# Optimization experiments

Hardware: AMD Instinct MI355X
Metric: run time of the kernel (lower is better)

## Reference

```python
import jax, jax.numpy as jnp
import numpy as np

T, H, I, E = 2048, 2048, 1024, 16
TOP_K = 4

def setup_inputs() -> dict:
    key = jax.random.key(0)
    k1, k2, k3, k4, k5 = jax.random.split(key, 5)
    scale = 0.02
    return {
        "hidden_states": jax.random.normal(k1, (T, H), dtype=jnp.float32),
        "gate_w": jax.random.normal(k2, (E, H), dtype=jnp.float32) * scale,
        "w1": jax.random.normal(k3, (E, H, I), dtype=jnp.float32) * scale,  # gate proj
        "w3": jax.random.normal(k4, (E, H, I), dtype=jnp.float32) * scale,  # up proj
        "w2": jax.random.normal(k5, (E, I, H), dtype=jnp.float32) * scale,  # down proj
    }

def reference(hidden_states, gate_w, w1, w3, w2):
    # Router gate in fp32 (ReplicatedLinear, params_dtype=fp32, no bias)
    logits = hidden_states.astype(jnp.float32) @ gate_w.T          # [T, E]
    scores = jax.nn.softmax(logits, axis=-1)                        # scoring_func=softmax
    topk_w, topk_idx = jax.lax.top_k(scores, TOP_K)                 # [T, K]
    # renormalize=True, routed_scaling_factor=1.0
    topk_w = topk_w / jnp.sum(topk_w, axis=-1, keepdims=True)
    # Dense combine weights [T, E]: zero for non-selected experts, so
    # the dense all-expert compute below is mathematically identical to
    # sparse dispatch + grouped GEMM + combine.
    tok = jnp.arange(T)[:, None]
    cw = jnp.zeros((T, E), jnp.float32).at[tok, topk_idx].add(topk_w)
    # SwiGLU expert MLPs
    h1 = jnp.einsum('th,ehi->eti', hidden_states, w1)               # [E, T, I]
    h3 = jnp.einsum('th,ehi->eti', hidden_states, w3)               # [E, T, I]
    h2 = jnp.einsum('eti,eih->eth', jax.nn.silu(h1) * h3, w2)       # [E, T, H]
    out = jnp.einsum('te,eth->th', cw.astype(hidden_states.dtype), h2)
    return out
```

## Files before the change

### kernel.cpp

```cpp
#include <hip/hip_runtime.h>
#include <hip/hip_bf16.h>
#include <math.h>

#define T_TOK 2048
#define H_DIM 2048
#define I_DIM 1024
#define E_NUM 16
#define TOPK  4

#define BM 128
#define BN 128
#define BK 32
#define MAXMB 80

typedef __attribute__((ext_vector_type(8))) __bf16 bf16x8;
typedef __attribute__((ext_vector_type(4))) float  f32x4;

__device__ __forceinline__ unsigned short f2bf(float f) {
    unsigned int u = __builtin_bit_cast(unsigned int, f);
    unsigned int r = u + 0x7FFFu + ((u >> 16) & 1u);
    return (unsigned short)(r >> 16);
}

__device__ __forceinline__ void gload16(const void* g, void* l) {
    __builtin_amdgcn_global_load_lds(
        (const __attribute__((address_space(1))) unsigned int*)g,
        (__attribute__((address_space(3))) unsigned int*)l,
        16, 0, 0);
}

static const size_t WS_COUNTS  = 0;
static const size_t WS_WORK    = 64;
static const size_t WS_OFFSETS = 256;
static const size_t WS_TOK     = 512;
static const size_t WS_WL      = 131584;
static const size_t WS_X16     = 262656;
static const size_t WS_W1T     = 8651264;
static const size_t WS_W3T     = 75760128;
static const size_t WS_W2T     = 142868992;
static const size_t WS_ACT     = 209977856;


__global__ void zero_init(float* __restrict__ out, int* __restrict__ counts) {
    int i = blockIdx.x * blockDim.x + threadIdx.x;
    ((float4*)out)[i] = make_float4(0.f, 0.f, 0.f, 0.f);
    if (i < E_NUM) counts[i] = 0;
}

__global__ void convert_x(const float* __restrict__ x, unsigned short* __restrict__ X16) {
    int i = blockIdx.x * blockDim.x + threadIdx.x;
    float4 v = ((const float4*)x)[i];
    ushort4 o;
    o.x = f2bf(v.x); o.y = f2bf(v.y); o.z = f2bf(v.z); o.w = f2bf(v.w);
    ((ushort4*)X16)[i] = o;
}

__global__ void transpose_conv(const float* __restrict__ in, unsigned short* __restrict__ out,
                               int R, int C) {
    __shared__ unsigned short tile[32][33];
    int e  = blockIdx.z;
    int c0 = blockIdx.x * 32;
    int r0 = blockIdx.y * 32;
    const float* ip = in + (size_t)e * R * C;
    unsigned short* op = out + (size_t)e * R * C;
    int t = threadIdx.x;
    int r  = t >> 3;
    int c4 = (t & 7) * 4;
    float4 v = *(const float4*)&ip[(size_t)(r0 + r) * C + c0 + c4];
    tile[c4 + 0][r] = f2bf(v.x);
    tile[c4 + 1][r] = f2bf(v.y);
    tile[c4 + 2][r] = f2bf(v.z);
    tile[c4 + 3][r] = f2bf(v.w);
    __syncthreads();
    ushort4 o;
    o.x = tile[r][c4 + 0];
    o.y = tile[r][c4 + 1];
    o.z = tile[r][c4 + 2];
    o.w = tile[r][c4 + 3];
    *(ushort4*)&op[(size_t)(c0 + r) * R + r0 + c4] = o;
}

__global__ void router(const float* __restrict__ x, const float* __restrict__ gw,
                       int* __restrict__ counts, int* __restrict__ tok,
                       float* __restrict__ wl) {
    int t = blockIdx.x;
    int lane = threadIdx.x;
    float acc[E_NUM];
#pragma unroll
    for (int e = 0; e < E_NUM; e++) acc[e] = 0.f;
    const float* xr = x + (size_t)t * H_DIM;
    for (int h = lane; h < H_DIM; h += 64) {
        float xv = xr[h];
#pragma unroll
        for (int e = 0; e < E_NUM; e++) acc[e] += xv * gw[e * H_DIM + h];
    }
#pragma unroll
    for (int e = 0; e < E_NUM; e++) {
#pragma unroll
        for (int off = 32; off; off >>= 1) acc[e] += __shfl_down(acc[e], off);
    }
    if (lane == 0) {
        bool used[E_NUM];
#pragma unroll
        for (int e = 0; e < E_NUM; e++) used[e] = false;
        int   idx[TOPK];
        float lv[TOPK];
        for (int k = 0; k < TOPK; k++) {
            float best = -1e30f; int bi = 0;
            for (int e = 0; e < E_NUM; e++)
                if (!used[e] && acc[e] > best) { best = acc[e]; bi = e; }
            used[bi] = true; idx[k] = bi; lv[k] = best;
        }
        float m = lv[0];
        float w[TOPK]; float s = 0.f;
        for (int k = 0; k < TOPK; k++) { w[k] = expf(lv[k] - m); s += w[k]; }
        float inv = 1.f / s;
        for (int k = 0; k < TOPK; k++) {
            int pos = atomicAdd(&counts[idx[k]], 1);
            tok[idx[k] * T_TOK + pos] = t;
            wl [idx[k] * T_TOK + pos] = w[k] * inv;
        }
    }
}

__global__ void prefix(const int* __restrict__ counts, int* __restrict__ offsets,
                       unsigned short* __restrict__ work) {
    if (threadIdx.x == 0 && blockIdx.x == 0) {
        int c[E_NUM]; int s = 0;
        for (int e = 0; e < E_NUM; e++) { c[e] = counts[e]; offsets[e] = s; s += c[e]; }
        offsets[E_NUM] = s;
        int n = 0;
        for (int e = 0; e < E_NUM; e++) {
            int mb = (c[e] + BM - 1) / BM;
            for (int m = 0; m < mb; m++) work[n++] = (unsigned short)((e << 8) | m);
        }
        offsets[E_NUM + 1] = n;
    }
}

__global__ __launch_bounds__(256, 2) void stage1(
    const unsigned short* __restrict__ X16,
    const unsigned short* __restrict__ w1t,
    const unsigned short* __restrict__ w3t,
    const int* __restrict__ offsets, const unsigned short* __restrict__ work,
    const int* __restrict__ tok, const float* __restrict__ wl,
    unsigned short* __restrict__ act)
{
    int j = blockIdx.y;
    if (j >= offsets[E_NUM + 1]) return;
    int ent = work[j];
    int e   = ent >> 8;
    int m0  = (ent & 255) * BM;
    int n_e = offsets[e + 1] - offsets[e];
    int n0  = blockIdx.x * BN;

    __shared__ __align__(16) unsigned short As [BM][BK];
    __shared__ __align__(16) unsigned short B1s[BN][BK];
    __shared__ __align__(16) unsigned short B2s[BN][BK];

    int tid  = threadIdx.x;
    int wave = tid >> 6, lane = tid & 63;
    int wm = (wave >> 1) * 64, wn = (wave & 1) * 64;
    int lr = lane & 15, lq = lane >> 4;

    const unsigned short* w1p = w1t + (size_t)e * I_DIM * H_DIM;
    const unsigned short* w3p = w3t + (size_t)e * I_DIM * H_DIM;

    int ar[2]; int rr[2]; int cc[2];
#pragma unroll
    for (int rep = 0; rep < 2; rep++) {
        int idx = rep * 256 + tid;
        rr[rep] = idx >> 2;
        cc[rep] = (idx & 3) * 8;
        int gm = m0 + rr[rep];
        ar[rep] = tok[e * T_TOK + (gm < n_e ? gm : n_e - 1)];
    }

    f32x4 acc1[4][4] = {};
    f32x4 acc3[4][4] = {};

    for (int k0 = 0; k0 < H_DIM; k0 += BK) {
#pragma unroll
        for (int rep = 0; rep < 2; rep++) {
            int r = rr[rep], ch = cc[rep];
            gload16(&X16[(size_t)ar[rep] * H_DIM + k0 + ch], &As [r][ch]);
            gload16(&w1p[(size_t)(n0 + r) * H_DIM + k0 + ch], &B1s[r][ch]);
            gload16(&w3p[(size_t)(n0 + r) * H_DIM + k0 + ch], &B2s[r][ch]);
        }
        __syncthreads();
        bf16x8 af[4], b1f[4], b2f[4];
#pragma unroll
        for (int ti = 0; ti < 4; ti++)
            af[ti] = *(const bf16x8*)&As[wm + ti * 16 + lr][lq * 8];
#pragma unroll
        for (int tj = 0; tj < 4; tj++) {
            b1f[tj] = *(const bf16x8*)&B1s[wn + tj * 16 + lr][lq * 8];
            b2f[tj] = *(const bf16x8*)&B2s[wn + tj * 16 + lr][lq * 8];
        }
#pragma unroll
        for (int ti = 0; ti < 4; ti++)
#pragma unroll
            for (int tj = 0; tj < 4; tj++) {
                acc1[ti][tj] = __builtin_amdgcn_mfma_f32_16x16x32_bf16(af[ti], b1f[tj], acc1[ti][tj], 0, 0, 0);
                acc3[ti][tj] = __builtin_amdgcn_mfma_f32_16x16x32_bf16(af[ti], b2f[tj], acc3[ti][tj], 0, 0, 0);
            }
        __syncthreads();
    }

    int slotbase = offsets[e] + m0;
#pragma unroll
    for (int ti = 0; ti < 4; ti++) {
#pragma unroll
        for (int reg = 0; reg < 4; reg++) {
            int mrow = wm + ti * 16 + lq * 4 + reg;
            int gm = m0 + mrow;
            if (gm >= n_e) continue;
            float wt = wl[e * T_TOK + gm];
            size_t obase = (size_t)(slotbase + mrow) * I_DIM + n0;
#pragma unroll
            for (int tj = 0; tj < 4; tj++) {
                float h1 = acc1[ti][tj][reg];
                float h3 = acc3[ti][tj][reg];
                float a = (h1 / (1.f + expf(-h1))) * h3 * wt;
                act[obase + wn + tj * 16 + lr] = f2bf(a);
            }
        }
    }
}

__global__ __launch_bounds__(256, 2) void stage2(
    const unsigned short* __restrict__ act,
    const unsigned short* __restrict__ w2t,
    const int* __restrict__ offsets, const unsigned short* __restrict__ work,
    const int* __restrict__ tok,
    float* __restrict__ out)
{
    int j = blockIdx.y;
    if (j >= offsets[E_NUM + 1]) return;
    int ent = work[j];
    int e   = ent >> 8;
    int m0  = (ent & 255) * BM;
    int n_e = offsets[e + 1] - offsets[e];
    int n0  = blockIdx.x * BN;

    __shared__ __align__(16) unsigned short As[BM][BK];
    __shared__ __align__(16) unsigned short Bs[BN][BK];

    int tid  = threadIdx.x;
    int wave = tid >> 6, lane = tid & 63;
    int wm = (wave >> 1) * 64, wn = (wave & 1) * 64;
    int lr = lane & 15, lq = lane >> 4;

    const unsigned short* w2p = w2t + (size_t)e * H_DIM * I_DIM;
    int slotbase = offsets[e];

    int rr[2]; int cc[2]; int arow[2];
#pragma unroll
    for (int rep = 0; rep < 2; rep++) {
        int idx = rep * 256 + tid;
        rr[rep] = idx >> 2;
        cc[rep] = (idx & 3) * 8;
        int gm = m0 + rr[rep];
        arow[rep] = slotbase + (gm < n_e ? gm : n_e - 1);
    }

    f32x4 acc[4][4] = {};

    for (int k0 = 0; k0 < I_DIM; k0 += BK) {
#pragma unroll
        for (int rep = 0; rep < 2; rep++) {
            int r = rr[rep], ch = cc[rep];
            gload16(&act[(size_t)arow[rep] * I_DIM + k0 + ch], &As[r][ch]);
            gload16(&w2p[(size_t)(n0 + r) * I_DIM + k0 + ch], &Bs[r][ch]);
        }
        __syncthreads();
        bf16x8 af[4], bf[4];
#pragma unroll
        for (int ti = 0; ti < 4; ti++)
            af[ti] = *(const bf16x8*)&As[wm + ti * 16 + lr][lq * 8];
#pragma unroll
        for (int tj = 0; tj < 4; tj++)
            bf[tj] = *(const bf16x8*)&Bs[wn + tj * 16 + lr][lq * 8];
#pragma unroll
        for (int ti = 0; ti < 4; ti++)
#pragma unroll
            for (int tj = 0; tj < 4; tj++)
                acc[ti][tj] = __builtin_amdgcn_mfma_f32_16x16x32_bf16(af[ti], bf[tj], acc[ti][tj], 0, 0, 0);
        __syncthreads();
    }

#pragma unroll
    for (int ti = 0; ti < 4; ti++) {
#pragma unroll
        for (int reg = 0; reg < 4; reg++) {
            int mrow = wm + ti * 16 + lq * 4 + reg;
            int gm = m0 + mrow;
            if (gm >= n_e) continue;
            int tm = tok[e * T_TOK + gm];
            size_t obase = (size_t)tm * H_DIM + n0;
#pragma unroll
            for (int tj = 0; tj < 4; tj++)
                atomicAdd(&out[obase + wn + tj * 16 + lr], acc[ti][tj][reg]);
        }
    }
}

extern "C" void kernel_launch(void* const* d_in, const int* in_sizes, int n_in,
                              void* d_out, int out_size, void* d_ws, size_t ws_size,
                              hipStream_t stream) {
    const float* x_f32 = (const float*)d_in[0];
    const float* gw    = (const float*)d_in[1];
    const float* w1    = (const float*)d_in[2];
    const float* w3    = (const float*)d_in[3];
    const float* w2    = (const float*)d_in[4];
    float* out = (float*)d_out;

    char* ws = (char*)d_ws;
    int*            counts  = (int*)(ws + WS_COUNTS);
    unsigned short* work    = (unsigned short*)(ws + WS_WORK);
    int*            offsets = (int*)(ws + WS_OFFSETS);
    int*            tok     = (int*)(ws + WS_TOK);
    float*          wl      = (float*)(ws + WS_WL);
    unsigned short* X16     = (unsigned short*)(ws + WS_X16);
    unsigned short* w1t     = (unsigned short*)(ws + WS_W1T);
    unsigned short* w3t     = (unsigned short*)(ws + WS_W3T);
    unsigned short* w2t     = (unsigned short*)(ws + WS_W2T);
    unsigned short* act     = (unsigned short*)(ws + WS_ACT);

    zero_init<<<dim3((T_TOK * H_DIM / 4) / 256), 256, 0, stream>>>(out, counts);
    convert_x<<<dim3((T_TOK * H_DIM / 4) / 256), 256, 0, stream>>>(x_f32, X16);
    transpose_conv<<<dim3(I_DIM / 32, H_DIM / 32, E_NUM), 256, 0, stream>>>(w1, w1t, H_DIM, I_DIM);
    transpose_conv<<<dim3(I_DIM / 32, H_DIM / 32, E_NUM), 256, 0, stream>>>(w3, w3t, H_DIM, I_DIM);
    transpose_conv<<<dim3(H_DIM / 32, I_DIM / 32, E_NUM), 256, 0, stream>>>(w2, w2t, I_DIM, H_DIM);
    router<<<dim3(T_TOK), 64, 0, stream>>>(x_f32, gw, counts, tok, wl);
    prefix<<<dim3(1), 64, 0, stream>>>(counts, offsets, work);
    stage1<<<dim3(I_DIM / BN, MAXMB), 256, 0, stream>>>(
        X16, w1t, w3t, offsets, work, tok, wl, act);
    stage2<<<dim3(H_DIM / BN, MAXMB), 256, 0, stream>>>(
        act, w2t, offsets, work, tok, out);
}
```

Baseline: 790.1 us.

## Replace atomic output scatter with slot buffer plus gather combine; widen transpose tiles

Stage2 now writes each expert's per-slot result into a dense fp32 scratch buffer (reusing the w1t region, which is dead after stage1) instead of atomically adding into the output. A new combine kernel sums each token's four slot rows, located through a posmap recorded by the router. This removes the 16M float atomics and the full zero-initialisation of the output, at the cost of an extra 64MB write and read through scratch. Separately, the weight transpose-convert kernel moves from 32x32 to 64x64 tiles with 16-byte vector stores, so each block does more work and writes are wider.

Result: faster. 767.7 us (-2.8%).

```diff
diff --git a/kernel.cpp b/kernel.cpp
--- a/kernel.cpp
+++ b/kernel.cpp
@@ -15,6 +15,7 @@
 
 typedef __attribute__((ext_vector_type(8))) __bf16 bf16x8;
 typedef __attribute__((ext_vector_type(4))) float  f32x4;
+typedef __attribute__((ext_vector_type(8))) unsigned short u16x8;
 
 __device__ __forceinline__ unsigned short f2bf(float f) {
     unsigned int u = __builtin_bit_cast(unsigned int, f);
@@ -36,15 +37,15 @@
 static const size_t WS_WL      = 131584;
 static const size_t WS_X16     = 262656;
 static const size_t WS_W1T     = 8651264;
+static const size_t WS_H2S     = 8651264;
 static const size_t WS_W3T     = 75760128;
 static const size_t WS_W2T     = 142868992;
 static const size_t WS_ACT     = 209977856;
-
-
-__global__ void zero_init(float* __restrict__ out, int* __restrict__ counts) {
-    int i = blockIdx.x * blockDim.x + threadIdx.x;
-    ((float4*)out)[i] = make_float4(0.f, 0.f, 0.f, 0.f);
-    if (i < E_NUM) counts[i] = 0;
+static const size_t WS_POSMAP  = 226755072;
+
+
+__global__ void zero_counts(int* __restrict__ counts) {
+    if (threadIdx.x < E_NUM) counts[threadIdx.x] = 0;
 }
 
 __global__ void convert_x(const float* __restrict__ x, unsigned short* __restrict__ X16) {
@@ -57,32 +58,40 @@
 
 __global__ void transpose_conv(const float* __restrict__ in, unsigned short* __restrict__ out,
                                int R, int C) {
-    __shared__ unsigned short tile[32][33];
+    __shared__ unsigned short tile[64][68];
     int e  = blockIdx.z;
-    int c0 = blockIdx.x * 32;
-    int r0 = blockIdx.y * 32;
+    int c0 = blockIdx.x * 64;
+    int r0 = blockIdx.y * 64;
     const float* ip = in + (size_t)e * R * C;
     unsigned short* op = out + (size_t)e * R * C;
-    int t = threadIdx.x;
-    int r  = t >> 3;
-    int c4 = (t & 7) * 4;
-    float4 v = *(const float4*)&ip[(size_t)(r0 + r) * C + c0 + c4];
-    tile[c4 + 0][r] = f2bf(v.x);
-    tile[c4 + 1][r] = f2bf(v.y);
-    tile[c4 + 2][r] = f2bf(v.z);
-    tile[c4 + 3][r] = f2bf(v.w);
+    int t  = threadIdx.x;
+    int rr = t >> 4;
+    int c4 = (t & 15) * 4;
+#pragma unroll
+    for (int p = 0; p < 4; p++) {
+        int r = p * 16 + rr;
+        float4 v = *(const float4*)&ip[(size_t)(r0 + r) * C + c0 + c4];
+        tile[c4 + 0][r] = f2bf(v.x);
+        tile[c4 + 1][r] = f2bf(v.y);
+        tile[c4 + 2][r] = f2bf(v.z);
+        tile[c4 + 3][r] = f2bf(v.w);
+    }
     __syncthreads();
-    ushort4 o;
-    o.x = tile[r][c4 + 0];
-    o.y = tile[r][c4 + 1];
-    o.z = tile[r][c4 + 2];
-    o.w = tile[r][c4 + 3];
-    *(ushort4*)&op[(size_t)(c0 + r) * R + r0 + c4] = o;
+    int cc = t >> 3;
+    int r8 = (t & 7) * 8;
+#pragma unroll
+    for (int p = 0; p < 2; p++) {
+        int c = p * 32 + cc;
+        union { u16x8 v8; ushort4 v4[2]; } u;
+        u.v4[0] = *(const ushort4*)&tile[c][r8];
+        u.v4[1] = *(const ushort4*)&tile[c][r8 + 4];
+        *(u16x8*)&op[(size_t)(c0 + c) * R + r0 + r8] = u.v8;
+    }
 }
 
 __global__ void router(const float* __restrict__ x, const float* __restrict__ gw,
                        int* __restrict__ counts, int* __restrict__ tok,
-                       float* __restrict__ wl) {
+                       float* __restrict__ wl, int* __restrict__ posmap) {
     int t = blockIdx.x;
     int lane = threadIdx.x;
     float acc[E_NUM];
@@ -119,6 +128,7 @@
             int pos = atomicAdd(&counts[idx[k]], 1);
             tok[idx[k] * T_TOK + pos] = t;
             wl [idx[k] * T_TOK + pos] = w[k] * inv;
+            posmap[t * TOPK + k] = (idx[k] << 16) | pos;
         }
     }
 }
@@ -232,8 +242,7 @@
     const unsigned short* __restrict__ act,
     const unsigned short* __restrict__ w2t,
     const int* __restrict__ offsets, const unsigned short* __restrict__ work,
-    const int* __restrict__ tok,
-    float* __restrict__ out)
+    float* __restrict__ h2s)
 {
     int j = blockIdx.y;
     if (j >= offsets[E_NUM + 1]) return;
@@ -296,13 +305,31 @@
             int mrow = wm + ti * 16 + lq * 4 + reg;
             int gm = m0 + mrow;
             if (gm >= n_e) continue;
-            int tm = tok[e * T_TOK + gm];
-            size_t obase = (size_t)tm * H_DIM + n0;
+            size_t obase = (size_t)(slotbase + gm) * H_DIM + n0;
 #pragma unroll
             for (int tj = 0; tj < 4; tj++)
-                atomicAdd(&out[obase + wn + tj * 16 + lr], acc[ti][tj][reg]);
-        }
-    }
+                h2s[obase + wn + tj * 16 + lr] = acc[ti][tj][reg];
+        }
+    }
+}
+
+__global__ void combine(const float* __restrict__ h2s, const int* __restrict__ posmap,
+                        const int* __restrict__ offsets, float* __restrict__ out) {
+    int t   = blockIdx.x;
+    int idx = blockIdx.y * 256 + threadIdx.x;
+    int slot[TOPK];
+#pragma unroll
+    for (int k = 0; k < TOPK; k++) {
+        int pm = posmap[t * TOPK + k];
+        slot[k] = offsets[pm >> 16] + (pm & 0xffff);
+    }
+    float4 s = make_float4(0.f, 0.f, 0.f, 0.f);
+#pragma unroll
+    for (int k = 0; k < TOPK; k++) {
+        float4 v = *(const float4*)&h2s[(size_t)slot[k] * H_DIM + idx * 4];
+        s.x += v.x; s.y += v.y; s.z += v.z; s.w += v.w;
+    }
+    *(float4*)&out[(size_t)t * H_DIM + idx * 4] = s;
 }
 
 extern "C" void kernel_launch(void* const* d_in, const int* in_sizes, int n_in,
@@ -323,19 +350,22 @@
     float*          wl      = (float*)(ws + WS_WL);
     unsigned short* X16     = (unsigned short*)(ws + WS_X16);
     unsigned short* w1t     = (unsigned short*)(ws + WS_W1T);
+    float*          h2s     = (float*)(ws + WS_H2S);
     unsigned short* w3t     = (unsigned short*)(ws + WS_W3T);
     unsigned short* w2t     = (unsigned short*)(ws + WS_W2T);
     unsigned short* act     = (unsigned short*)(ws + WS_ACT);
-
-    zero_init<<<dim3((T_TOK * H_DIM / 4) / 256), 256, 0, stream>>>(out, counts);
+    int*            posmap  = (int*)(ws + WS_POSMAP);
+
+    zero_counts<<<dim3(1), 64, 0, stream>>>(counts);
     convert_x<<<dim3((T_TOK * H_DIM / 4) / 256), 256, 0, stream>>>(x_f32, X16);
-    transpose_conv<<<dim3(I_DIM / 32, H_DIM / 32, E_NUM), 256, 0, stream>>>(w1, w1t, H_DIM, I_DIM);
-    transpose_conv<<<dim3(I_DIM / 32, H_DIM / 32, E_NUM), 256, 0, stream>>>(w3, w3t, H_DIM, I_DIM);
-    transpose_conv<<<dim3(H_DIM / 32, I_DIM / 32, E_NUM), 256, 0, stream>>>(w2, w2t, I_DIM, H_DIM);
-    router<<<dim3(T_TOK), 64, 0, stream>>>(x_f32, gw, counts, tok, wl);
+    transpose_conv<<<dim3(I_DIM / 64, H_DIM / 64, E_NUM), 256, 0, stream>>>(w1, w1t, H_DIM, I_DIM);
+    transpose_conv<<<dim3(I_DIM / 64, H_DIM / 64, E_NUM), 256, 0, stream>>>(w3, w3t, H_DIM, I_DIM);
+    transpose_conv<<<dim3(H_DIM / 64, I_DIM / 64, E_NUM), 256, 0, stream>>>(w2, w2t, I_DIM, H_DIM);
+    router<<<dim3(T_TOK), 64, 0, stream>>>(x_f32, gw, counts, tok, wl, posmap);
     prefix<<<dim3(1), 64, 0, stream>>>(counts, offsets, work);
     stage1<<<dim3(I_DIM / BN, MAXMB), 256, 0, stream>>>(
         X16, w1t, w3t, offsets, work, tok, wl, act);
     stage2<<<dim3(H_DIM / BN, MAXMB), 256, 0, stream>>>(
-        act, w2t, offsets, work, tok, out);
-}
+        act, w2t, offsets, work, h2s);
+    combine<<<dim3(T_TOK, 2), 256, 0, stream>>>(h2s, posmap, offsets, out);
+}
```
